# Optimization experiments

Hardware: AMD Instinct MI355X
Metric: run time of the kernel (lower is better)

Reference implementation:

```python
import jax, jax.numpy as jnp
import numpy as np

B, S, D_IN, D_ATT = 8, 2048, 512, 512

def setup_inputs() -> dict:
    key = jax.random.key(0)
    ks = jax.random.split(key, 7)
    sc = 1.0 / np.sqrt(D_IN)
    return {
        "x": jax.random.normal(ks[0], (B, S, D_IN), dtype=jnp.float32),
        "Wq": jax.random.uniform(ks[1], (D_IN, D_ATT), jnp.float32, -sc, sc),
        "bq": jax.random.uniform(ks[2], (D_ATT,), jnp.float32, -sc, sc),
        "Wk": jax.random.uniform(ks[3], (D_IN, D_ATT), jnp.float32, -sc, sc),
        "bk": jax.random.uniform(ks[4], (D_ATT,), jnp.float32, -sc, sc),
        "Wv": jax.random.uniform(ks[5], (D_IN, D_ATT), jnp.float32, -sc, sc),
        "bv": jax.random.uniform(ks[6], (D_ATT,), jnp.float32, -sc, sc),
    }

def reference(x, Wq, bq, Wk, bk, Wv, bv):
    # Linear projections: [B, S, D_att]
    q = jnp.einsum("bsd,de->bse", x, Wq) + bq
    k = jnp.einsum("bsd,de->bse", x, Wk) + bk
    v = jnp.einsum("bsd,de->bse", x, Wv) + bv
    # Full scores matrix [B, S, S]; note: NO 1/sqrt(d) scaling in original.
    scores = jnp.einsum("bqe,bke->bqk", q, k)
    attn = jax.nn.softmax(scores, axis=-1)
    return jnp.einsum("bqk,bke->bqe", attn, v)
```

## Files before the change

### kernel.cpp

```cpp
#include <hip/hip_runtime.h>
#include <cstdint>
#include <cstddef>


#define SEQ 2048
#define DIM 512
#define NB 8
#define BSZ (NB * SEQ)
#define KT 64
#define NT (SEQ / KT)

typedef __attribute__((ext_vector_type(8))) _Float16 half8;
typedef __attribute__((ext_vector_type(2))) __fp16 fp16x2;
typedef __attribute__((ext_vector_type(4))) float f32x4;
typedef __attribute__((ext_vector_type(16))) float f32x16;

__device__ __forceinline__ unsigned short f2h(float f) {
  _Float16 h = (_Float16)f;
  return __builtin_bit_cast(unsigned short, h);
}
__device__ __forceinline__ half8 ld_frag(const unsigned short* p) {
  return *(const half8*)(const void*)p;
}
__device__ __forceinline__ void gl_lds16(const unsigned short* g, unsigned short* l) {
  __builtin_amdgcn_global_load_lds(
      (__attribute__((address_space(1))) void*)g,
      (__attribute__((address_space(3))) void*)l, 16, 0, 0);
}
__device__ __forceinline__ void bar_vm0() {
  asm volatile("s_waitcnt vmcnt(0)\ns_barrier" ::: "memory");
}
__device__ __forceinline__ void bar_lgkm() {
  asm volatile("s_waitcnt lgkmcnt(0)\ns_barrier" ::: "memory");
}
__device__ __forceinline__ void bar_lgkm_vm0() {
  asm volatile("s_waitcnt lgkmcnt(0) vmcnt(0)\ns_barrier" ::: "memory");
}

__global__ __launch_bounds__(256) void cvt_x_kernel(
    const float* __restrict__ X, unsigned short* __restrict__ xh)
{
  size_t i0 = ((size_t)blockIdx.x * 256 + threadIdx.x) * 8;
  float4 a = *(const float4*)&X[i0];
  float4 b = *(const float4*)&X[i0 + 4];
  ushort4 o0; o0.x = f2h(a.x); o0.y = f2h(a.y); o0.z = f2h(a.z); o0.w = f2h(a.w);
  ushort4 o1; o1.x = f2h(b.x); o1.y = f2h(b.y); o1.z = f2h(b.z); o1.w = f2h(b.w);
  *(ushort4*)&xh[i0] = o0;
  *(ushort4*)&xh[i0 + 4] = o1;
}

__global__ __launch_bounds__(256) void cvt_w_kernel(
    const float* __restrict__ Wq, const float* __restrict__ Wk,
    const float* __restrict__ Wv, unsigned short* __restrict__ Wt)
{
  const int z = blockIdx.z;
  const float* W = (z == 0) ? Wq : (z == 1) ? Wk : Wv;
  unsigned short* out = Wt + (size_t)z * DIM * DIM;
  const int k0 = blockIdx.x * 64, n0 = blockIdx.y * 64;
  const int t = threadIdx.x;
  __shared__ unsigned short tl[64 * 72];
#pragma unroll
  for (int i = 0; i < 4; i++) {
    int f = t + 256 * i;
    int kr = f >> 4, c4 = (f & 15) * 4;
    float4 v = *(const float4*)&W[(size_t)(k0 + kr) * DIM + n0 + c4];
    tl[(c4 + 0) * 72 + kr] = f2h(v.x);
    tl[(c4 + 1) * 72 + kr] = f2h(v.y);
    tl[(c4 + 2) * 72 + kr] = f2h(v.z);
    tl[(c4 + 3) * 72 + kr] = f2h(v.w);
  }
  __syncthreads();
#pragma unroll
  for (int i = 0; i < 2; i++) {
    int f = t + 256 * i;
    int nr = f >> 3, k8 = (f & 7) * 8;
    *(uint4*)&out[(size_t)(n0 + nr) * DIM + k0 + k8] = *(const uint4*)&tl[nr * 72 + k8];
  }
}

__global__ __launch_bounds__(256) void proj_kernel(
    const unsigned short* __restrict__ xh, const unsigned short* __restrict__ Wt,
    const float* __restrict__ bq, const float* __restrict__ bk,
    const float* __restrict__ bv, unsigned short* __restrict__ outbase)
{
  const int z = blockIdx.z;
  const unsigned short* Wz = Wt + (size_t)z * DIM * DIM;
  const float* bias = (z == 0) ? bq : (z == 1) ? bk : bv;
  unsigned short* out = outbase + (size_t)z * BSZ * DIM;
  const int m0 = blockIdx.x * 128, n0 = blockIdx.y * 128;
  const int t = threadIdx.x, lane = t & 63, wave = t >> 6;
  const int wrow = (wave >> 1) * 64, wcol = (wave & 1) * 64;
  const int lr = lane & 15, lq = (lane >> 4) * 8;

  __shared__ unsigned short sm[128 * 132];
  unsigned short* As = sm;
  unsigned short* Bs = sm + 128 * 64;

  f32x4 acc[4][4];
  const f32x4 zero = {0.f, 0.f, 0.f, 0.f};
#pragma unroll
  for (int r = 0; r < 4; r++)
#pragma unroll
    for (int c = 0; c < 4; c++) acc[r][c] = zero;

  for (int k0 = 0; k0 < DIM; k0 += 64) {
    __syncthreads();
#pragma unroll
    for (int i = 0; i < 4; i++) {
      int f = t + 256 * i;
      int row = f >> 3, c8 = (f & 7) * 8;
      gl_lds16(&xh[(size_t)(m0 + row) * DIM + k0 + c8], &As[i * 2048 + wave * 512]);
      gl_lds16(&Wz[(size_t)(n0 + row) * DIM + k0 + c8], &Bs[i * 2048 + wave * 512]);
    }
    __syncthreads();
#pragma unroll
    for (int kk = 0; kk < 64; kk += 32) {
      half8 a[4], b[4];
#pragma unroll
      for (int r = 0; r < 4; r++) a[r] = ld_frag(&As[(wrow + 16 * r + lr) * 64 + kk + lq]);
#pragma unroll
      for (int c = 0; c < 4; c++) b[c] = ld_frag(&Bs[(wcol + 16 * c + lr) * 64 + kk + lq]);
#pragma unroll
      for (int r = 0; r < 4; r++)
#pragma unroll
        for (int c = 0; c < 4; c++)
          acc[r][c] = __builtin_amdgcn_mfma_f32_16x16x32_f16(a[r], b[c], acc[r][c], 0, 0, 0);
    }
  }
  __syncthreads();
#pragma unroll
  for (int c = 0; c < 4; c++) {
    float bb = bias[n0 + wcol + 16 * c + lr];
#pragma unroll
    for (int r = 0; r < 4; r++)
#pragma unroll
      for (int e = 0; e < 4; e++)
        sm[(wrow + 16 * r + (lane >> 4) * 4 + e) * 132 + wcol + 16 * c + lr] =
            f2h(acc[r][c][e] + bb);
  }
  __syncthreads();
#pragma unroll
  for (int i = 0; i < 8; i++) {
    int f = t + 256 * i;
    int row = f >> 4, c8 = (f & 15) * 8;
    *(uint4*)&out[(size_t)(m0 + row) * DIM + n0 + c8] = *(const uint4*)&sm[row * 132 + c8];
  }
}

__global__ __launch_bounds__(256) void vtrans_kernel(
    const unsigned short* __restrict__ vh, unsigned short* __restrict__ vt)
{
  const int b = blockIdx.z;
  const int s0 = blockIdx.x * 64, n0 = blockIdx.y * 64;
  const int t = threadIdx.x;
  __shared__ unsigned short tl[64 * 72];
#pragma unroll
  for (int i = 0; i < 2; i++) {
    int f = t + 256 * i;
    int sr = f >> 3, c8 = (f & 7) * 8;
    uint4 raw = *(const uint4*)&vh[((size_t)b * SEQ + s0 + sr) * DIM + n0 + c8];
    unsigned short u[8];
    *(uint4*)u = raw;
#pragma unroll
    for (int j = 0; j < 8; j++) tl[(c8 + j) * 72 + sr] = u[j];
  }
  __syncthreads();
#pragma unroll
  for (int i = 0; i < 2; i++) {
    int f = t + 256 * i;
    int nr = f >> 3, s8 = (f & 7) * 8;
    *(uint4*)&vt[((size_t)b * DIM + n0 + nr) * SEQ + s0 + s8] = *(const uint4*)&tl[nr * 72 + s8];
  }
}

#define PSTR 72
#define OSTR 516

__global__ __launch_bounds__(256, 1) void flash_kernel(
    const unsigned short* __restrict__ Qb, const unsigned short* __restrict__ Kb,
    const unsigned short* __restrict__ Vtb, float* __restrict__ Ob)
{
  const int zb = blockIdx.x & 7;
  const int q0 = (blockIdx.x >> 3) * 64;
  const unsigned short* Q = Qb + (size_t)zb * SEQ * DIM;
  const unsigned short* K = Kb + (size_t)zb * SEQ * DIM;
  const unsigned short* V = Vtb + (size_t)zb * DIM * SEQ;
  float* Out = Ob + (size_t)zb * SEQ * DIM;

  const int t = threadIdx.x, lane = t & 63, wave = t >> 6;
  const int l31 = lane & 31, hi = lane >> 5;
  const int kh = wave & 1, rh = wave >> 1;
  const int lr = lane & 15, lq4 = lane >> 4;
  const float L2E = 1.4426950408889634f;

  __shared__ unsigned short lds[70912];
  unsigned short* Qbuf = lds;
  unsigned short* Kbuf = lds + 32768;
  unsigned short* Pbuf = lds + 65536;
  float* mpart = (float*)(lds + 65536 + 64 * PSTR);
  float* lpart = mpart + 128;
  float* abuf = lpart + 128;
  float* lrun = abuf + 64;

  if (t < 64) lrun[t] = 0.f;

  int koff[16];
#pragma unroll
  for (int i = 0; i < 16; i++) {
    int f = t + 256 * i;
    int row = f >> 6, c = f & 63;
    koff[i] = row * DIM + (c ^ (row & 7)) * 8;
  }

#pragma unroll
  for (int i = 0; i < 16; i++)
    gl_lds16(&Q[(size_t)q0 * DIM + koff[i]], &Qbuf[i * 2048 + wave * 512]);
#pragma unroll
  for (int i = 0; i < 16; i++)
    gl_lds16(&K[koff[i]], &Kbuf[i * 2048 + wave * 512]);

  f32x4 acc[32];
  const f32x4 zero = {0.f, 0.f, 0.f, 0.f};
#pragma unroll
  for (int ob = 0; ob < 32; ob++) acc[ob] = zero;
  float m_run = -__builtin_inff();

  const int keyrow = kh * 32 + l31, ksw = keyrow & 7;
  const int qrow = rh * 32 + l31, qsw = qrow & 7;
  const unsigned short* Kc = Kbuf + keyrow * 512;
  const unsigned short* Qc = Qbuf + qrow * 512;

  for (int kt = 0; kt < NT; kt++) {
    bar_vm0();

    const unsigned short* Vb = V + (size_t)(wave * 128 + lr) * SEQ + kt * KT + lq4 * 8;
    half8 vfA[8];
#pragma unroll
    for (int dc = 0; dc < 4; dc++)
#pragma unroll
      for (int ks = 0; ks < 2; ks++)
        vfA[dc * 2 + ks] = ld_frag(Vb + (size_t)dc * 16 * SEQ + ks * 32);

    f32x16 s0 = {0.f, 0.f, 0.f, 0.f, 0.f, 0.f, 0.f, 0.f,
                 0.f, 0.f, 0.f, 0.f, 0.f, 0.f, 0.f, 0.f};
    f32x16 s1 = s0;
    __builtin_amdgcn_s_setprio(1);
#pragma unroll
    for (int j = 0; j < 16; j++) {
      half8 kf0 = ld_frag(&Kc[((2 * j + hi) ^ ksw) << 3]);
      half8 qv0 = ld_frag(&Qc[((2 * j + hi) ^ qsw) << 3]);
      half8 kf1 = ld_frag(&Kc[((2 * (j + 16) + hi) ^ ksw) << 3]);
      half8 qv1 = ld_frag(&Qc[((2 * (j + 16) + hi) ^ qsw) << 3]);
      s0 = __builtin_amdgcn_mfma_f32_32x32x16_f16(kf0, qv0, s0, 0, 0, 0);
      s1 = __builtin_amdgcn_mfma_f32_32x32x16_f16(kf1, qv1, s1, 0, 0, 0);
    }
    __builtin_amdgcn_s_setprio(0);
    f32x16 sacc = s0 + s1;

    float mx = sacc[0];
#pragma unroll
    for (int i2 = 1; i2 < 16; i2++) mx = fmaxf(mx, sacc[i2]);
    mx = fmaxf(mx, __shfl_xor(mx, 32, 64));
    if (lane < 32) mpart[kh * 64 + rh * 32 + lane] = mx;
    bar_lgkm();

    half8 vfB[8];
#pragma unroll
    for (int dc = 0; dc < 4; dc++)
#pragma unroll
      for (int ks = 0; ks < 2; ks++)
        vfB[dc * 2 + ks] = ld_frag(Vb + (size_t)(dc + 4) * 16 * SEQ + ks * 32);
    if (kt + 1 < NT) {
      const unsigned short* Kt = K + (size_t)(kt + 1) * KT * DIM;
#pragma unroll
      for (int i = 0; i < 16; i++)
        gl_lds16(&Kt[koff[i]], &Kbuf[i * 2048 + wave * 512]);
    }

    float mo = mpart[(kh ^ 1) * 64 + rh * 32 + l31];
    float mnew = fmaxf(m_run, fmaxf(mx, mo));
    float alpha = exp2f((m_run - mnew) * L2E);
    m_run = mnew;
    if (kh == 0 && lane < 32) abuf[rh * 32 + lane] = alpha;
    float psum = 0.f;
#pragma unroll
    for (int w = 0; w < 8; w++) {
      float p0 = exp2f((sacc[2 * w] - mnew) * L2E);
      float p1 = exp2f((sacc[2 * w + 1] - mnew) * L2E);
      psum += p0 + p1;
      fp16x2 pk = __builtin_amdgcn_cvt_pkrtz(p0, p1);
      int keyoff = (w >> 1) * 8 + (w & 1) * 2 + 4 * hi;
      *(unsigned int*)&Pbuf[qrow * PSTR + kh * 32 + keyoff] =
          __builtin_bit_cast(unsigned int, pk);
    }
    psum += __shfl_xor(psum, 32, 64);
    if (lane < 32) lpart[kh * 64 + rh * 32 + lane] = psum;
    bar_lgkm();
    if (kh == 0 && lane < 32) {
      int r = rh * 32 + lane;
      lrun[r] = alpha * lrun[r] + lpart[r] + lpart[64 + r];
    }

#pragma unroll
    for (int rg = 0; rg < 4; rg++)
#pragma unroll
      for (int e = 0; e < 4; e++) {
        float a = abuf[rg * 16 + lq4 * 4 + e];
#pragma unroll
        for (int dc = 0; dc < 8; dc++) acc[rg * 8 + dc][e] *= a;
      }

    half8 pf[4][2];
#pragma unroll
    for (int rg = 0; rg < 4; rg++)
#pragma unroll
      for (int ks = 0; ks < 2; ks++)
        pf[rg][ks] = ld_frag(&Pbuf[(rg * 16 + lr) * PSTR + ks * 32 + lq4 * 8]);
    __builtin_amdgcn_s_setprio(1);
#pragma unroll
    for (int dc = 0; dc < 4; dc++)
#pragma unroll
      for (int rg = 0; rg < 4; rg++) {
        acc[rg * 8 + dc] =
            __builtin_amdgcn_mfma_f32_16x16x32_f16(pf[rg][0], vfA[dc * 2 + 0],
                                                   acc[rg * 8 + dc], 0, 0, 0);
        acc[rg * 8 + dc] =
            __builtin_amdgcn_mfma_f32_16x16x32_f16(pf[rg][1], vfA[dc * 2 + 1],
                                                   acc[rg * 8 + dc], 0, 0, 0);
      }
#pragma unroll
    for (int dc = 4; dc < 8; dc++)
#pragma unroll
      for (int rg = 0; rg < 4; rg++) {
        acc[rg * 8 + dc] =
            __builtin_amdgcn_mfma_f32_16x16x32_f16(pf[rg][0], vfB[(dc - 4) * 2 + 0],
                                                   acc[rg * 8 + dc], 0, 0, 0);
        acc[rg * 8 + dc] =
            __builtin_amdgcn_mfma_f32_16x16x32_f16(pf[rg][1], vfB[(dc - 4) * 2 + 1],
                                                   acc[rg * 8 + dc], 0, 0, 0);
      }
    __builtin_amdgcn_s_setprio(0);
  }

  bar_lgkm_vm0();

  float linv[4][4];
#pragma unroll
  for (int rg = 0; rg < 4; rg++)
#pragma unroll
    for (int e = 0; e < 4; e++) linv[rg][e] = 1.0f / lrun[rg * 16 + lq4 * 4 + e];

  float* Obuf = (float*)lds;
#pragma unroll
  for (int h = 0; h < 2; h++) {
    __syncthreads();
#pragma unroll
    for (int r2 = 0; r2 < 2; r2++) {
      int rg = h * 2 + r2;
#pragma unroll
      for (int e = 0; e < 4; e++) {
        int rowh = r2 * 16 + lq4 * 4 + e;
#pragma unroll
        for (int dc = 0; dc < 8; dc++)
          Obuf[rowh * OSTR + wave * 128 + dc * 16 + lr] = acc[rg * 8 + dc][e] * linv[rg][e];
      }
    }
    __syncthreads();
#pragma unroll
    for (int i = 0; i < 16; i++) {
      int f = t + 256 * i;
      int rowh = f >> 7, c4 = (f & 127) * 4;
      *(float4*)&Out[(size_t)(q0 + h * 32 + rowh) * DIM + c4] =
          *(const float4*)&Obuf[rowh * OSTR + c4];
    }
  }
}

extern "C" void kernel_launch(void* const* d_in, const int* in_sizes, int n_in,
                              void* d_out, int out_size, void* d_ws, size_t ws_size,
                              hipStream_t stream)
{
  const float* X  = (const float*)d_in[0];
  const float* Wq = (const float*)d_in[1];
  const float* bq = (const float*)d_in[2];
  const float* Wk = (const float*)d_in[3];
  const float* bk = (const float*)d_in[4];
  const float* Wv = (const float*)d_in[5];
  const float* bv = (const float*)d_in[6];
  float* Out = (float*)d_out;

  char* ws = (char*)d_ws;
  const size_t MB = 1u << 20;
  unsigned short* qh = (unsigned short*)(ws);
  unsigned short* kh = (unsigned short*)(ws + 16 * MB);
  unsigned short* vh = (unsigned short*)(ws + 32 * MB);
  unsigned short* vt = (unsigned short*)(ws + 48 * MB);
  unsigned short* xh = (unsigned short*)(ws + 48 * MB);
  unsigned short* Wt = (unsigned short*)(ws + 64 * MB);

  cvt_x_kernel<<<dim3(BSZ * DIM / 2048), 256, 0, stream>>>(X, xh);
  cvt_w_kernel<<<dim3(8, 8, 3), 256, 0, stream>>>(Wq, Wk, Wv, Wt);
  proj_kernel<<<dim3(BSZ / 128, DIM / 128, 3), 256, 0, stream>>>(
      xh, Wt, bq, bk, bv, qh);
  vtrans_kernel<<<dim3(SEQ / 64, DIM / 64, NB), 256, 0, stream>>>(vh, vt);
  flash_kernel<<<dim3(NB * SEQ / 64), 256, 0, stream>>>(qh, kh, vt, Out);
}
```

Before: 306.5 us.

## Skip online-softmax rescale when max growth is small; pad P buffer and vectorize stores

Adds a lazy rescaling threshold: the running max is kept unless the new tile max exceeds it by more than 8, and a per-wave ballot flag lets the block skip the accumulator rescale loop when every row keeps its max. P stores are widened to 64-bit writes and the P row stride is changed to 68, with reads split into two 64-bit loads, to reduce LDS bank conflicts. The next-K prefetch is issued before the V fragment loads. Exponentials may now reach up to e^8 before being written as fp16, which narrows the numeric headroom.

New measurement: 293.2 us. -4.4%, faster.

```diff
diff --git a/kernel.cpp b/kernel.cpp
--- a/kernel.cpp
+++ b/kernel.cpp
@@ -11,6 +11,7 @@
 #define NT (SEQ / KT)
 
 typedef __attribute__((ext_vector_type(8))) _Float16 half8;
+typedef __attribute__((ext_vector_type(4))) _Float16 half4;
 typedef __attribute__((ext_vector_type(2))) __fp16 fp16x2;
 typedef __attribute__((ext_vector_type(4))) float f32x4;
 typedef __attribute__((ext_vector_type(16))) float f32x16;
@@ -173,7 +174,7 @@
   }
 }
 
-#define PSTR 72
+#define PSTR 68
 #define OSTR 516
 
 __global__ __launch_bounds__(256, 1) void flash_kernel(
@@ -193,7 +194,7 @@
   const int lr = lane & 15, lq4 = lane >> 4;
   const float L2E = 1.4426950408889634f;
 
-  __shared__ unsigned short lds[70912];
+  __shared__ unsigned short lds[70664];
   unsigned short* Qbuf = lds;
   unsigned short* Kbuf = lds + 32768;
   unsigned short* Pbuf = lds + 65536;
@@ -201,6 +202,7 @@
   float* lpart = mpart + 128;
   float* abuf = lpart + 128;
   float* lrun = abuf + 64;
+  unsigned int* fbuf = (unsigned int*)(lrun + 64);
 
   if (t < 64) lrun[t] = 0.f;
 
@@ -264,34 +266,43 @@
     if (lane < 32) mpart[kh * 64 + rh * 32 + lane] = mx;
     bar_lgkm();
 
+    if (kt + 1 < NT) {
+      const unsigned short* Kt = K + (size_t)(kt + 1) * KT * DIM;
+#pragma unroll
+      for (int i = 0; i < 16; i++)
+        gl_lds16(&Kt[koff[i]], &Kbuf[i * 2048 + wave * 512]);
+    }
     half8 vfB[8];
 #pragma unroll
     for (int dc = 0; dc < 4; dc++)
 #pragma unroll
       for (int ks = 0; ks < 2; ks++)
         vfB[dc * 2 + ks] = ld_frag(Vb + (size_t)(dc + 4) * 16 * SEQ + ks * 32);
-    if (kt + 1 < NT) {
-      const unsigned short* Kt = K + (size_t)(kt + 1) * KT * DIM;
-#pragma unroll
-      for (int i = 0; i < 16; i++)
-        gl_lds16(&Kt[koff[i]], &Kbuf[i * 2048 + wave * 512]);
-    }
 
     float mo = mpart[(kh ^ 1) * 64 + rh * 32 + l31];
-    float mnew = fmaxf(m_run, fmaxf(mx, mo));
-    float alpha = exp2f((m_run - mnew) * L2E);
+    float mxc = fmaxf(mx, mo);
+    bool keep = (mxc - m_run <= 8.0f);
+    float mnew = keep ? m_run : mxc;
+    float alpha = keep ? 1.0f : exp2f((m_run - mnew) * L2E);
     m_run = mnew;
     if (kh == 0 && lane < 32) abuf[rh * 32 + lane] = alpha;
+    unsigned long long ball = __ballot(keep);
+    if (lane == 0) fbuf[wave] = (ball == ~0ull) ? 1u : 0u;
+
     float psum = 0.f;
 #pragma unroll
-    for (int w = 0; w < 8; w++) {
-      float p0 = exp2f((sacc[2 * w] - mnew) * L2E);
-      float p1 = exp2f((sacc[2 * w + 1] - mnew) * L2E);
-      psum += p0 + p1;
-      fp16x2 pk = __builtin_amdgcn_cvt_pkrtz(p0, p1);
-      int keyoff = (w >> 1) * 8 + (w & 1) * 2 + 4 * hi;
-      *(unsigned int*)&Pbuf[qrow * PSTR + kh * 32 + keyoff] =
-          __builtin_bit_cast(unsigned int, pk);
+    for (int w2 = 0; w2 < 4; w2++) {
+      float p0 = exp2f((sacc[4 * w2 + 0] - mnew) * L2E);
+      float p1 = exp2f((sacc[4 * w2 + 1] - mnew) * L2E);
+      float p2 = exp2f((sacc[4 * w2 + 2] - mnew) * L2E);
+      float p3 = exp2f((sacc[4 * w2 + 3] - mnew) * L2E);
+      psum += (p0 + p1) + (p2 + p3);
+      fp16x2 pa = __builtin_amdgcn_cvt_pkrtz(p0, p1);
+      fp16x2 pb = __builtin_amdgcn_cvt_pkrtz(p2, p3);
+      unsigned long long both =
+          ((unsigned long long)__builtin_bit_cast(unsigned int, pb) << 32) |
+          __builtin_bit_cast(unsigned int, pa);
+      *(unsigned long long*)&Pbuf[qrow * PSTR + kh * 32 + w2 * 8 + 4 * hi] = both;
     }
     psum += __shfl_xor(psum, 32, 64);
     if (lane < 32) lpart[kh * 64 + rh * 32 + lane] = psum;
@@ -301,21 +312,30 @@
       lrun[r] = alpha * lrun[r] + lpart[r] + lpart[64 + r];
     }
 
+    if (!(fbuf[0] & fbuf[1] & fbuf[2] & fbuf[3])) {
+#pragma unroll
+      for (int rg = 0; rg < 4; rg++)
+#pragma unroll
+        for (int e = 0; e < 4; e++) {
+          float a = abuf[rg * 16 + lq4 * 4 + e];
+#pragma unroll
+          for (int dc = 0; dc < 8; dc++) acc[rg * 8 + dc][e] *= a;
+        }
+    }
+
+    half8 pf[4][2];
 #pragma unroll
     for (int rg = 0; rg < 4; rg++)
 #pragma unroll
-      for (int e = 0; e < 4; e++) {
-        float a = abuf[rg * 16 + lq4 * 4 + e];
-#pragma unroll
-        for (int dc = 0; dc < 8; dc++) acc[rg * 8 + dc][e] *= a;
+      for (int ks = 0; ks < 2; ks++) {
+        const unsigned short* pp = &Pbuf[(rg * 16 + lr) * PSTR + ks * 32 + lq4 * 8];
+        half4 lo = *(const half4*)(const void*)pp;
+        half4 h2 = *(const half4*)(const void*)(pp + 4);
+        half8 v;
+#pragma unroll
+        for (int q = 0; q < 4; q++) { v[q] = lo[q]; v[4 + q] = h2[q]; }
+        pf[rg][ks] = v;
       }
-
-    half8 pf[4][2];
-#pragma unroll
-    for (int rg = 0; rg < 4; rg++)
-#pragma unroll
-      for (int ks = 0; ks < 2; ks++)
-        pf[rg][ks] = ld_frag(&Pbuf[(rg * 16 + lr) * PSTR + ks * 32 + lq4 * 8]);
     __builtin_amdgcn_s_setprio(1);
 #pragma unroll
     for (int dc = 0; dc < 4; dc++)
```
